# Optimization experiments

Hardware: AMD Instinct MI355X
Metric: run time of the kernel (lower is better)

Reference implementation:

```python
import jax, jax.numpy as jnp
import numpy as np

B, N, NONGT, D, H, PE = 128, 36, 36, 1024, 16, 64
DG = D // H  # per-head dim = 64


def setup_inputs() -> dict:
    key = jax.random.key(0)
    ks = jax.random.split(key, 10)
    s = 0.02
    return {
        "roi_feat": jax.random.normal(ks[0], (B, N, D), jnp.float32),
        "adj_matrix": jax.random.randint(ks[1], (B, N, NONGT), 0, 2, jnp.int32),
        "position_embedding": jax.random.normal(ks[2], (B, N, NONGT, PE), jnp.float32),
        "label_biases_att": jax.random.normal(ks[3], (B, N, NONGT), jnp.float32) * 0.1,
        # effective (weight-normed) linear weights
        "Wq": jax.random.normal(ks[4], (D, D), jnp.float32) * s,
        "bq": jnp.zeros((D,), jnp.float32),
        "Wk": jax.random.normal(ks[5], (D, D), jnp.float32) * s,
        "bk": jnp.zeros((D,), jnp.float32),
        "Wpos": jax.random.normal(ks[6], (H, PE), jnp.float32) * s,
        "bpos": jnp.zeros((H,), jnp.float32),
        # grouped 1x1 conv (groups=H): per-head projection feat_dim -> feat_dim/H
        "Wout": jax.random.normal(ks[7], (H, DG, D), jnp.float32) * s,
        "bout": jnp.zeros((D,), jnp.float32),
    }


def reference(roi_feat, adj_matrix, position_embedding, label_biases_att,
              Wq, bq, Wk, bk, Wpos, bpos, Wout, bout):
    b, n, d = roi_feat.shape
    nongt = adj_matrix.shape[2]
    dg = d // H
    v = roi_feat[:, :nongt, :]                                  # [B,nongt,D]
    q = (roi_feat @ Wq.T + bq).reshape(b, n, H, dg)             # [B,N,H,dg]
    k = (v @ Wk.T + bk).reshape(b, nongt, H, dg)                # [B,nongt,H,dg]
    # scaled QK^T, laid out [B,N,H,nongt] (orig: matmul then transpose(1,2))
    aff = jnp.einsum('bnhd,bmhd->bnhm', q, k) / jnp.sqrt(jnp.float32(dg))
    # position log-bias
    pos = jax.nn.relu(position_embedding.reshape(b, n * nongt, -1) @ Wpos.T + bpos)
    pos = pos.reshape(b, n, nongt, H).transpose(0, 1, 3, 2)     # [B,N,H,nongt]
    waff = aff + jnp.log(jnp.maximum(pos, jnp.float32(1e-6)))
    # adjacency mask + label bias (orig does this in [B,N,nongt,H] layout; equivalent)
    mask = adj_matrix[:, :, None, :] > 0                        # [B,N,1,nongt]
    waff = jnp.where(mask, waff, jnp.float32(-9e15)) + label_biases_att[:, :, None, :]
    att = jax.nn.softmax(waff, axis=-1)                         # [B,N,H,nongt]
    # weighted sum of full V (note: V is full feat_dim per head, not dg)
    out_t = jnp.einsum('bnhm,bmd->bnhd', att, v)                # [B,N,H,D]
    # grouped 1x1 conv: per-head D -> D/H, heads concatenated
    out = jnp.einsum('bnhd,hed->bnhe', out_t, Wout).reshape(b, n, d) + bout
    return out
```

## Files before the change

kernel.cpp:

```cpp
#include <hip/hip_runtime.h>
#include <hip/hip_bf16.h>

#define BB 128
#define NN 36
#define DD 1024
#define HH 16
#define ROWS (BB*NN)

typedef __attribute__((ext_vector_type(8))) __bf16 bf16x8;
typedef __attribute__((ext_vector_type(4))) float f32x4;
typedef __attribute__((ext_vector_type(4))) unsigned short us4;

__device__ inline unsigned short f2bf(float f) {
    __hip_bfloat16 h = __float2bfloat16(f);
    return *reinterpret_cast<unsigned short*>(&h);
}

__device__ inline void async16(const unsigned short* g, unsigned short* l) {
    __builtin_amdgcn_global_load_lds((const __attribute__((address_space(1))) unsigned int*)g,
                                     (__attribute__((address_space(3))) unsigned int*)l, 16, 0, 0);
}

__global__ __launch_bounds__(256) void prep_kernel(const float* __restrict__ roi,
                                                   const float* __restrict__ Wq,
                                                   const float* __restrict__ Wk,
                                                   const float* __restrict__ Wout,
                                                   const float* __restrict__ pe,
                                                   const float* __restrict__ Wpos,
                                                   const float* __restrict__ bpos,
                                                   const int* __restrict__ adj,
                                                   const float* __restrict__ lbl,
                                                   unsigned short* __restrict__ roi_bf,
                                                   unsigned short* __restrict__ Wcat_bf,
                                                   float* __restrict__ extra) {
    const int bid = blockIdx.x, tid = threadIdx.x;
    if (bid < 4608) {
        int i = bid * 256 + tid;
        f32x4 v = ((const f32x4*)roi)[i];
        us4 o;
        o.x = f2bf(v[0]); o.y = f2bf(v[1]); o.z = f2bf(v[2]); o.w = f2bf(v[3]);
        ((us4*)roi_bf)[i] = o;
        return;
    }
    if (bid < 7680) {
        int wb = bid - 4608;
        int sel = wb >> 10;
        const float* src = sel == 0 ? Wq : (sel == 1 ? Wk : Wout);
        int i = (wb & 1023) * 256 + tid;
        f32x4 v = ((const f32x4*)src)[i];
        us4 o;
        o.x = f2bf(v[0]); o.y = f2bf(v[1]); o.z = f2bf(v[2]); o.w = f2bf(v[3]);
        ((us4*)(Wcat_bf + (size_t)sel * DD * DD))[i] = o;
        return;
    }
    __shared__ __align__(16) float wps[HH * 64];
    __shared__ float bps[HH];
    for (int i = tid; i < HH * 64; i += 256) wps[i] = Wpos[i];
    if (tid < HH) bps[tid] = bpos[tid];
    __syncthreads();

    int idx = (bid - 7680) * 256 + tid;
    f32x4 pr[16];
    const f32x4* pv = (const f32x4*)(pe + (size_t)idx * 64);
#pragma unroll
    for (int j = 0; j < 16; j++) pr[j] = pv[j];
    int a = adj[idx];
    float add = lbl[idx] + (a > 0 ? 0.f : -9e15f);
    int b = idx / 1296, nm = idx % 1296;
    size_t obase = (size_t)b * (16 * 1296) + nm;
    for (int hh = 0; hh < 16; hh++) {
        const f32x4* wv = (const f32x4*)(wps + hh * 64);
        f32x4 acc4 = {0.f, 0.f, 0.f, 0.f};
#pragma unroll
        for (int j = 0; j < 16; j++) acc4 += pr[j] * wv[j];
        float d = acc4[0] + acc4[1] + acc4[2] + acc4[3] + bps[hh];
        d = fmaxf(d, 0.f);
        d = __logf(fmaxf(d, 1e-6f));
        extra[obase + (size_t)hh * 1296] = d + add;
    }
}

__global__ __launch_bounds__(256, 2) void fused_kernel(const unsigned short* __restrict__ A,
                                                       const unsigned short* __restrict__ Wc,
                                                       const float* __restrict__ bq,
                                                       const float* __restrict__ bk,
                                                       const float* __restrict__ extra,
                                                       const float* __restrict__ bout,
                                                       float* __restrict__ out) {
    __shared__ __align__(16) unsigned short pool[21504];
    const int tid  = threadIdx.x;
    const int wave = tid >> 6, lane = tid & 63;
    const int quad = lane >> 4, l16 = lane & 15;
    const int h  = blockIdx.x & 15;
    const int bg = blockIdx.x >> 4;
    const int row0 = bg * 144;

    unsigned short* As = pool;
    unsigned short* Bs = pool + 9216;

    const unsigned short* gsrc[11];
    unsigned short* ldst[11];
#pragma unroll
    for (int i = 0; i < 11; i++) {
        int j = wave + 4 * i;
        int c = j * 64 + lane;
        if (j < 18) {
            int row = c >> 3;
            int col = ((c & 7) ^ (row & 7)) * 8;
            gsrc[i] = A + (size_t)(row0 + row) * DD + col;
            ldst[i] = As + j * 512;
        } else {
            int cb = c - 1152;
            int row = cb >> 3;
            int sec = row >> 6;
            int wrow = sec * DD + h * 64 + (row & 63);
            int col = ((cb & 7) ^ (row & 7)) * 8;
            gsrc[i] = Wc + (size_t)wrow * DD + col;
            ldst[i] = Bs + (j - 18) * 512;
        }
    }

    f32x4 acc[9][3] = {};

#pragma unroll
    for (int k0i = 0; k0i < 16; k0i++) {
#pragma unroll
        for (int i = 0; i < 11; i++) {
            if (i < 10 || wave < 2)
                async16(gsrc[i] + k0i * 64, ldst[i]);
        }
        __syncthreads();

#pragma unroll
        for (int ks = 0; ks < 2; ks++) {
            int kch = ks * 4 + quad;
            bf16x8 bfv[3], afv[9];
#pragma unroll
            for (int ct = 0; ct < 3; ct++) {
                int rowb = wave * 48 + ct * 16 + l16;
                bfv[ct] = *(const bf16x8*)&Bs[rowb * 64 + ((kch ^ (rowb & 7)) * 8)];
            }
#pragma unroll
            for (int rt = 0; rt < 9; rt++) {
                int rowa = rt * 16 + l16;
                afv[rt] = *(const bf16x8*)&As[rowa * 64 + ((kch ^ (rowa & 7)) * 8)];
            }
#pragma unroll
            for (int rt = 0; rt < 9; rt++)
#pragma unroll
                for (int ct = 0; ct < 3; ct++)
                    acc[rt][ct] = __builtin_amdgcn_mfma_f32_16x16x32_bf16(afv[rt], bfv[ct], acc[rt][ct], 0, 0, 0);
        }
        __syncthreads();
    }

    const int bat = wave;
    const float* exb = extra + ((size_t)((bg * 4 + bat) * 16 + h)) * 1296;
    float exv[3][4][3];
#pragma unroll
    for (int mt = 0; mt < 3; mt++)
#pragma unroll
        for (int r = 0; r < 4; r++) {
            int row = mt * 16 + quad * 4 + r;
#pragma unroll
            for (int nt = 0; nt < 3; nt++) {
                int col = nt * 16 + l16;
                exv[mt][r][nt] = (row < 36 && col < 36) ? exb[row * 36 + col] : 0.f;
            }
        }
    float bo[4];
#pragma unroll
    for (int nt = 0; nt < 4; nt++) bo[nt] = bout[h * 64 + nt * 16 + l16];

    unsigned short* qL = pool;
    unsigned short* kL = pool + 10368;
#pragma unroll
    for (int ct = 0; ct < 3; ct++) {
        int g = wave * 48 + ct * 16 + l16;
        int sec = g >> 6, e = g & 63;
        if (sec < 2) {
            unsigned short* dst = (sec == 0) ? qL : kL;
            float bias = (sec == 0) ? bq[h * 64 + e] : bk[h * 64 + e];
#pragma unroll
            for (int rt = 0; rt < 9; rt++)
#pragma unroll
                for (int r = 0; r < 4; r++) {
                    int row = rt * 16 + quad * 4 + r;
                    dst[row * 72 + e] = f2bf(acc[rt][ct][r] + bias);
                }
        }
    }
    __syncthreads();

    const unsigned short* qB = qL + bat * 36 * 72;
    const unsigned short* kB = kL + bat * 36 * 72;
    int rq[3];
#pragma unroll
    for (int t = 0; t < 3; t++) { int rr = t * 16 + l16; rq[t] = rr < 36 ? rr : 35; }

    f32x4 aff[3][3] = {};
#pragma unroll
    for (int ks = 0; ks < 2; ks++) {
        bf16x8 afr[3], bfr[3];
#pragma unroll
        for (int t = 0; t < 3; t++) afr[t] = *(const bf16x8*)&qB[rq[t] * 72 + ks * 32 + quad * 8];
#pragma unroll
        for (int t = 0; t < 3; t++) bfr[t] = *(const bf16x8*)&kB[rq[t] * 72 + ks * 32 + quad * 8];
#pragma unroll
        for (int mt = 0; mt < 3; mt++)
#pragma unroll
            for (int nt = 0; nt < 3; nt++)
                aff[mt][nt] = __builtin_amdgcn_mfma_f32_16x16x32_bf16(afr[mt], bfr[nt], aff[mt][nt], 0, 0, 0);
    }
    __syncthreads();

    unsigned short* vwT   = pool;
    unsigned short* attsL = pool + 10240 + bat * 2688;
#pragma unroll
    for (int mt = 0; mt < 3; mt++) {
#pragma unroll
        for (int r = 0; r < 4; r++) {
            int row = mt * 16 + quad * 4 + r;
            float w[3];
#pragma unroll
            for (int nt = 0; nt < 3; nt++) {
                int col = nt * 16 + l16;
                bool valid = (row < 36) && (col < 36);
                w[nt] = valid ? (aff[mt][nt][r] * 0.125f + exv[mt][r][nt]) : -3.4e38f;
            }
            float mx = fmaxf(fmaxf(w[0], w[1]), w[2]);
#pragma unroll
            for (int d = 1; d < 16; d <<= 1) mx = fmaxf(mx, __shfl_xor(mx, d));
            float e0 = __expf(w[0] - mx), e1 = __expf(w[1] - mx), e2 = __expf(w[2] - mx);
            float s = e0 + e1 + e2;
#pragma unroll
            for (int d = 1; d < 16; d <<= 1) s += __shfl_xor(s, d);
            float rs = 1.0f / s;
            attsL[row * 56 + 0  + l16] = f2bf(e0 * rs);
            attsL[row * 56 + 16 + l16] = f2bf(e1 * rs);
            attsL[row * 56 + 32 + l16] = f2bf(e2 * rs);
        }
    }
#pragma unroll
    for (int ct = 0; ct < 3; ct++) {
        int g = wave * 48 + ct * 16 + l16;
        int sec = g >> 6, e = g & 63;
        if (sec == 2) {
#pragma unroll
            for (int rt = 0; rt < 9; rt++)
#pragma unroll
                for (int r = 0; r < 4; r++) {
                    int row = rt * 16 + quad * 4 + r;
                    int bb = row / 36, m = row - bb * 36;
                    vwT[bb * 2560 + e * 40 + m] = f2bf(acc[rt][ct][r]);
                }
        }
    }
    __syncthreads();

    const unsigned short* vB = vwT + bat * 2560;
    f32x4 o[3][4] = {};
    {
        bf16x8 pa[3], pb[4], zf = {};
#pragma unroll
        for (int mt = 0; mt < 3; mt++) pa[mt] = *(const bf16x8*)&attsL[(mt * 16 + l16) * 56 + quad * 8];
#pragma unroll
        for (int nt = 0; nt < 4; nt++) pb[nt] = *(const bf16x8*)&vB[(nt * 16 + l16) * 40 + quad * 8];
#pragma unroll
        for (int mt = 0; mt < 3; mt++)
#pragma unroll
            for (int nt = 0; nt < 4; nt++)
                o[mt][nt] = __builtin_amdgcn_mfma_f32_16x16x32_bf16(pa[mt], pb[nt], o[mt][nt], 0, 0, 0);
#pragma unroll
        for (int mt = 0; mt < 3; mt++)
            pa[mt] = (quad < 2) ? *(const bf16x8*)&attsL[(mt * 16 + l16) * 56 + 32 + quad * 8] : zf;
#pragma unroll
        for (int nt = 0; nt < 4; nt++)
            pb[nt] = (quad < 2) ? *(const bf16x8*)&vB[(nt * 16 + l16) * 40 + 32 + quad * 8] : zf;
#pragma unroll
        for (int mt = 0; mt < 3; mt++)
#pragma unroll
            for (int nt = 0; nt < 4; nt++)
                o[mt][nt] = __builtin_amdgcn_mfma_f32_16x16x32_bf16(pa[mt], pb[nt], o[mt][nt], 0, 0, 0);
    }

    const size_t obase = (size_t)((bg * 4 + bat) * 36) * DD + h * 64;
#pragma unroll
    for (int mt = 0; mt < 3; mt++)
#pragma unroll
        for (int r = 0; r < 4; r++) {
            int n = mt * 16 + quad * 4 + r;
            if (n < 36) {
#pragma unroll
                for (int nt = 0; nt < 4; nt++)
                    out[obase + (size_t)n * DD + nt * 16 + l16] = o[mt][nt][r] + bo[nt];
            }
        }
}

extern "C" void kernel_launch(void* const* d_in, const int* in_sizes, int n_in,
                              void* d_out, int out_size, void* d_ws, size_t ws_size,
                              hipStream_t stream) {
    const float* roi  = (const float*)d_in[0];
    const int*   adj  = (const int*)  d_in[1];
    const float* pe   = (const float*)d_in[2];
    const float* lbl  = (const float*)d_in[3];
    const float* Wq   = (const float*)d_in[4];
    const float* bq   = (const float*)d_in[5];
    const float* Wk   = (const float*)d_in[6];
    const float* bk   = (const float*)d_in[7];
    const float* Wpos = (const float*)d_in[8];
    const float* bpos = (const float*)d_in[9];
    const float* Wout = (const float*)d_in[10];
    const float* bout = (const float*)d_in[11];
    float* out = (float*)d_out;

    char* w = (char*)d_ws;
    unsigned short* roi_bf  = (unsigned short*)(w);
    unsigned short* Wcat_bf = (unsigned short*)(w + 9437184);
    float*          extra   = (float*)(w + 15728640);

    prep_kernel<<<8328, 256, 0, stream>>>(roi, Wq, Wk, Wout, pe, Wpos, bpos, adj, lbl,
                                          roi_bf, Wcat_bf, extra);
    fused_kernel<<<32 * 16, 256, 0, stream>>>(roi_bf, Wcat_bf, bq, bk, extra, bout, out);
}
```

Measured before the change: 173.0 us.

## Double-buffer GEMM main loop with 512-thread blocks covering 8 batches

Each block grows from 256 to 512 threads and now covers 288 rows (8 batches) instead of 144, so the grid halves to 256 blocks. The K loop switches from single-buffer load-sync-compute to double-buffered LDS. Prefetches of the next tile are interleaved with MFMA phases, and the loop uses barriers, waitcnt and s_setprio scheduling hints. The goal is to hide global-to-LDS latency and reuse the weight tile across more rows, at the cost of much larger LDS use and fewer blocks.

Result: slower. 186.9 us (+8.0%).

```diff
diff --git a/kernel.cpp b/kernel.cpp
--- a/kernel.cpp
+++ b/kernel.cpp
@@ -80,82 +80,128 @@
     }
 }
 
-__global__ __launch_bounds__(256, 2) void fused_kernel(const unsigned short* __restrict__ A,
+__global__ __launch_bounds__(512, 2) void fused_kernel(const unsigned short* __restrict__ A,
                                                        const unsigned short* __restrict__ Wc,
                                                        const float* __restrict__ bq,
                                                        const float* __restrict__ bk,
                                                        const float* __restrict__ extra,
                                                        const float* __restrict__ bout,
                                                        float* __restrict__ out) {
-    __shared__ __align__(16) unsigned short pool[21504];
+    __shared__ __align__(16) unsigned short pool[61440];
     const int tid  = threadIdx.x;
     const int wave = tid >> 6, lane = tid & 63;
     const int quad = lane >> 4, l16 = lane & 15;
     const int h  = blockIdx.x & 15;
     const int bg = blockIdx.x >> 4;
-    const int row0 = bg * 144;
-
-    unsigned short* As = pool;
-    unsigned short* Bs = pool + 9216;
-
-    const unsigned short* gsrc[11];
-    unsigned short* ldst[11];
-#pragma unroll
-    for (int i = 0; i < 11; i++) {
-        int j = wave + 4 * i;
-        int c = j * 64 + lane;
-        if (j < 18) {
+    const int row0 = bg * 288;
+    const int wm = wave >> 2, wn = wave & 3;
+    const bool tail = (wave < 4);
+
+    const unsigned short* gsrc[8];
+    int loff[8];
+#pragma unroll
+    for (int i = 0; i < 8; i++) {
+        int j = wave + 8 * i;
+        int jj = j < 60 ? j : 0;
+        int c = jj * 64 + lane;
+        if (jj < 36) {
             int row = c >> 3;
             int col = ((c & 7) ^ (row & 7)) * 8;
             gsrc[i] = A + (size_t)(row0 + row) * DD + col;
-            ldst[i] = As + j * 512;
+            loff[i] = jj * 512;
         } else {
-            int cb = c - 1152;
+            int cb = c - 2304;
             int row = cb >> 3;
             int sec = row >> 6;
             int wrow = sec * DD + h * 64 + (row & 63);
             int col = ((cb & 7) ^ (row & 7)) * 8;
             gsrc[i] = Wc + (size_t)wrow * DD + col;
-            ldst[i] = Bs + (j - 18) * 512;
+            loff[i] = 18432 + (jj - 36) * 512;
         }
     }
 
     f32x4 acc[9][3] = {};
 
 #pragma unroll
-    for (int k0i = 0; k0i < 16; k0i++) {
-#pragma unroll
-        for (int i = 0; i < 11; i++) {
-            if (i < 10 || wave < 2)
-                async16(gsrc[i] + k0i * 64, ldst[i]);
-        }
-        __syncthreads();
-
-#pragma unroll
-        for (int ks = 0; ks < 2; ks++) {
-            int kch = ks * 4 + quad;
-            bf16x8 bfv[3], afv[9];
-#pragma unroll
-            for (int ct = 0; ct < 3; ct++) {
-                int rowb = wave * 48 + ct * 16 + l16;
-                bfv[ct] = *(const bf16x8*)&Bs[rowb * 64 + ((kch ^ (rowb & 7)) * 8)];
-            }
-#pragma unroll
-            for (int rt = 0; rt < 9; rt++) {
-                int rowa = rt * 16 + l16;
-                afv[rt] = *(const bf16x8*)&As[rowa * 64 + ((kch ^ (rowa & 7)) * 8)];
-            }
-#pragma unroll
-            for (int rt = 0; rt < 9; rt++)
-#pragma unroll
-                for (int ct = 0; ct < 3; ct++)
-                    acc[rt][ct] = __builtin_amdgcn_mfma_f32_16x16x32_bf16(afv[rt], bfv[ct], acc[rt][ct], 0, 0, 0);
-        }
-        __syncthreads();
-    }
+    for (int i = 0; i < 7; i++) async16(gsrc[i], pool + loff[i]);
+    if (tail) async16(gsrc[7], pool + loff[7]);
+    asm volatile("s_waitcnt vmcnt(0)" ::: "memory");
+    __builtin_amdgcn_s_barrier();
+
+#define LDB(ct_, kch_) { int rowb = wn * 48 + (ct_) * 16 + l16; \
+    bfv[ct_] = *(const bf16x8*)&cbuf[18432 + rowb * 64 + (((kch_) ^ (rowb & 7)) * 8)]; }
+#define LDA(rt_, kch_) { int rowa = wm * 144 + (rt_) * 16 + l16; \
+    afv[rt_] = *(const bf16x8*)&cbuf[rowa * 64 + (((kch_) ^ (rowa & 7)) * 8)]; }
+#define STAGE(i_) { if ((i_) < 7 || tail) async16(gsrc[i_] + kadv, nbuf + loff[i_]); }
+#define PH_WAIT { __builtin_amdgcn_s_barrier(); \
+    asm volatile("s_waitcnt lgkmcnt(0)" ::: "memory"); \
+    __builtin_amdgcn_sched_barrier(0); }
+
+#pragma unroll 2
+    for (int t = 0; t < 16; ++t) {
+        unsigned short* cbuf = pool + (t & 1) * 30720;
+        unsigned short* nbuf = pool + ((t & 1) ^ 1) * 30720;
+        const int kadv = (t + 1) * 64;
+        const bool pf = (t < 15);
+        bf16x8 bfv[3], afv[9];
+
+        LDB(0, quad) LDB(1, quad) LDB(2, quad)
+        LDA(0, quad) LDA(1, quad) LDA(2, quad) LDA(3, quad) LDA(4, quad)
+        if (pf) { STAGE(0) STAGE(1) STAGE(2) }
+        PH_WAIT;
+        __builtin_amdgcn_s_setprio(1);
+#pragma unroll
+        for (int rt = 0; rt < 5; rt++)
+#pragma unroll
+            for (int ct = 0; ct < 3; ct++)
+                acc[rt][ct] = __builtin_amdgcn_mfma_f32_16x16x32_bf16(afv[rt], bfv[ct], acc[rt][ct], 0, 0, 0);
+        __builtin_amdgcn_s_setprio(0);
+        __builtin_amdgcn_s_barrier();
+
+        LDA(5, quad) LDA(6, quad) LDA(7, quad) LDA(8, quad)
+        if (pf) { STAGE(3) STAGE(4) STAGE(5) }
+        PH_WAIT;
+        __builtin_amdgcn_s_setprio(1);
+#pragma unroll
+        for (int rt = 5; rt < 9; rt++)
+#pragma unroll
+            for (int ct = 0; ct < 3; ct++)
+                acc[rt][ct] = __builtin_amdgcn_mfma_f32_16x16x32_bf16(afv[rt], bfv[ct], acc[rt][ct], 0, 0, 0);
+        __builtin_amdgcn_s_setprio(0);
+        __builtin_amdgcn_s_barrier();
+
+        LDB(0, 4 + quad) LDB(1, 4 + quad) LDB(2, 4 + quad)
+        LDA(0, 4 + quad) LDA(1, 4 + quad) LDA(2, 4 + quad) LDA(3, 4 + quad) LDA(4, 4 + quad)
+        if (pf) { STAGE(6) STAGE(7) }
+        PH_WAIT;
+        __builtin_amdgcn_s_setprio(1);
+#pragma unroll
+        for (int rt = 0; rt < 5; rt++)
+#pragma unroll
+            for (int ct = 0; ct < 3; ct++)
+                acc[rt][ct] = __builtin_amdgcn_mfma_f32_16x16x32_bf16(afv[rt], bfv[ct], acc[rt][ct], 0, 0, 0);
+        __builtin_amdgcn_s_setprio(0);
+        __builtin_amdgcn_s_barrier();
+
+        LDA(5, 4 + quad) LDA(6, 4 + quad) LDA(7, 4 + quad) LDA(8, 4 + quad)
+        PH_WAIT;
+        __builtin_amdgcn_s_setprio(1);
+#pragma unroll
+        for (int rt = 5; rt < 9; rt++)
+#pragma unroll
+            for (int ct = 0; ct < 3; ct++)
+                acc[rt][ct] = __builtin_amdgcn_mfma_f32_16x16x32_bf16(afv[rt], bfv[ct], acc[rt][ct], 0, 0, 0);
+        __builtin_amdgcn_s_setprio(0);
+        asm volatile("s_waitcnt vmcnt(0)" ::: "memory");
+        __builtin_amdgcn_s_barrier();
+    }
+#undef LDB
+#undef LDA
+#undef STAGE
+#undef PH_WAIT
 
     const int bat = wave;
-    const float* exb = extra + ((size_t)((bg * 4 + bat) * 16 + h)) * 1296;
+    const float* exb = extra + ((size_t)((bg * 8 + bat) * 16 + h)) * 1296;
     float exv[3][4][3];
 #pragma unroll
     for (int mt = 0; mt < 3; mt++)
@@ -173,10 +219,10 @@
     for (int nt = 0; nt < 4; nt++) bo[nt] = bout[h * 64 + nt * 16 + l16];
 
     unsigned short* qL = pool;
-    unsigned short* kL = pool + 10368;
+    unsigned short* kL = pool + 20736;
 #pragma unroll
     for (int ct = 0; ct < 3; ct++) {
-        int g = wave * 48 + ct * 16 + l16;
+        int g = wn * 48 + ct * 16 + l16;
         int sec = g >> 6, e = g & 63;
         if (sec < 2) {
             unsigned short* dst = (sec == 0) ? qL : kL;
@@ -185,7 +231,7 @@
             for (int rt = 0; rt < 9; rt++)
 #pragma unroll
                 for (int r = 0; r < 4; r++) {
-                    int row = rt * 16 + quad * 4 + r;
+                    int row = wm * 144 + rt * 16 + quad * 4 + r;
                     dst[row * 72 + e] = f2bf(acc[rt][ct][r] + bias);
                 }
         }
@@ -215,7 +261,7 @@
     __syncthreads();
 
     unsigned short* vwT   = pool;
-    unsigned short* attsL = pool + 10240 + bat * 2688;
+    unsigned short* attsL = pool + 20480 + bat * 2688;
 #pragma unroll
     for (int mt = 0; mt < 3; mt++) {
 #pragma unroll
@@ -243,14 +289,14 @@
     }
 #pragma unroll
     for (int ct = 0; ct < 3; ct++) {
-        int g = wave * 48 + ct * 16 + l16;
+        int g = wn * 48 + ct * 16 + l16;
         int sec = g >> 6, e = g & 63;
         if (sec == 2) {
 #pragma unroll
             for (int rt = 0; rt < 9; rt++)
 #pragma unroll
                 for (int r = 0; r < 4; r++) {
-                    int row = rt * 16 + quad * 4 + r;
+                    int row = wm * 144 + rt * 16 + quad * 4 + r;
                     int bb = row / 36, m = row - bb * 36;
                     vwT[bb * 2560 + e * 40 + m] = f2bf(acc[rt][ct][r]);
                 }
@@ -284,7 +330,7 @@
                 o[mt][nt] = __builtin_amdgcn_mfma_f32_16x16x32_bf16(pa[mt], pb[nt], o[mt][nt], 0, 0, 0);
     }
 
-    const size_t obase = (size_t)((bg * 4 + bat) * 36) * DD + h * 64;
+    const size_t obase = (size_t)((bg * 8 + bat) * 36) * DD + h * 64;
 #pragma unroll
     for (int mt = 0; mt < 3; mt++)
 #pragma unroll
@@ -322,5 +368,5 @@
 
     prep_kernel<<<8328, 256, 0, stream>>>(roi, Wq, Wk, Wout, pe, Wpos, bpos, adj, lbl,
                                           roi_bf, Wcat_bf, extra);
-    fused_kernel<<<32 * 16, 256, 0, stream>>>(roi_bf, Wcat_bf, bq, bk, extra, bout, out);
-}
+    fused_kernel<<<16 * 16, 512, 0, stream>>>(roi_bf, Wcat_bf, bq, bk, extra, bout, out);
+}
```

## Double-buffer GEMM K-loop with 32-wide K tiles and async prefetch

Applied to the files above, without the earlier changes.

The main GEMM loop moves from single-buffered 64-wide K tiles, which synchronised twice per step and stalled on every load, to double-buffered 32-wide K tiles. The next tile is issued with async global-to-LDS loads while MFMAs run on the current one. The LDS swizzle is adapted to the narrower rows, and s_setprio is raised around the MFMA block. The cost is twice as many iterations and barriers, and it relies on the 32-wide layout being conflict-free.

Result: faster. 168.6 us (-2.6%).

```diff
diff --git a/kernel.cpp b/kernel.cpp
--- a/kernel.cpp
+++ b/kernel.cpp
@@ -95,62 +95,64 @@
     const int bg = blockIdx.x >> 4;
     const int row0 = bg * 144;
 
-    unsigned short* As = pool;
-    unsigned short* Bs = pool + 9216;
-
-    const unsigned short* gsrc[11];
-    unsigned short* ldst[11];
-#pragma unroll
-    for (int i = 0; i < 11; i++) {
+    const unsigned short* gsrc[6];
+    int loff[6];
+#pragma unroll
+    for (int i = 0; i < 6; i++) {
         int j = wave + 4 * i;
-        int c = j * 64 + lane;
-        if (j < 18) {
-            int row = c >> 3;
-            int col = ((c & 7) ^ (row & 7)) * 8;
+        int jj = j < 21 ? j : 0;
+        int c = jj * 64 + lane;
+        if (jj < 9) {
+            int row = c >> 2, cc = c & 3;
+            int col = (cc ^ ((row >> 1) & 3)) * 8;
             gsrc[i] = A + (size_t)(row0 + row) * DD + col;
-            ldst[i] = As + j * 512;
+            loff[i] = jj * 512;
         } else {
-            int cb = c - 1152;
-            int row = cb >> 3;
+            int cb = c - 576;
+            int row = cb >> 2, cc = cb & 3;
             int sec = row >> 6;
             int wrow = sec * DD + h * 64 + (row & 63);
-            int col = ((cb & 7) ^ (row & 7)) * 8;
+            int col = (cc ^ ((row >> 1) & 3)) * 8;
             gsrc[i] = Wc + (size_t)wrow * DD + col;
-            ldst[i] = Bs + (j - 18) * 512;
+            loff[i] = 4608 + (jj - 9) * 512;
         }
     }
 
     f32x4 acc[9][3] = {};
 
 #pragma unroll
-    for (int k0i = 0; k0i < 16; k0i++) {
-#pragma unroll
-        for (int i = 0; i < 11; i++) {
-            if (i < 10 || wave < 2)
-                async16(gsrc[i] + k0i * 64, ldst[i]);
-        }
-        __syncthreads();
-
-#pragma unroll
-        for (int ks = 0; ks < 2; ks++) {
-            int kch = ks * 4 + quad;
-            bf16x8 bfv[3], afv[9];
-#pragma unroll
-            for (int ct = 0; ct < 3; ct++) {
-                int rowb = wave * 48 + ct * 16 + l16;
-                bfv[ct] = *(const bf16x8*)&Bs[rowb * 64 + ((kch ^ (rowb & 7)) * 8)];
-            }
-#pragma unroll
-            for (int rt = 0; rt < 9; rt++) {
-                int rowa = rt * 16 + l16;
-                afv[rt] = *(const bf16x8*)&As[rowa * 64 + ((kch ^ (rowa & 7)) * 8)];
-            }
-#pragma unroll
-            for (int rt = 0; rt < 9; rt++)
-#pragma unroll
-                for (int ct = 0; ct < 3; ct++)
-                    acc[rt][ct] = __builtin_amdgcn_mfma_f32_16x16x32_bf16(afv[rt], bfv[ct], acc[rt][ct], 0, 0, 0);
-        }
+    for (int i = 0; i < 6; i++)
+        if (i < 5 || wave == 0) async16(gsrc[i], pool + loff[i]);
+    __syncthreads();
+
+#pragma unroll 2
+    for (int t = 0; t < 32; ++t) {
+        unsigned short* cbuf = pool + (t & 1) * 10752;
+        unsigned short* nbuf = pool + ((t & 1) ^ 1) * 10752;
+        if (t < 31) {
+            const int kadv = (t + 1) * 32;
+#pragma unroll
+            for (int i = 0; i < 6; i++)
+                if (i < 5 || wave == 0) async16(gsrc[i] + kadv, nbuf + loff[i]);
+        }
+        bf16x8 bfv[3], afv[9];
+#pragma unroll
+        for (int ct = 0; ct < 3; ct++) {
+            int rowb = wave * 48 + ct * 16 + l16;
+            bfv[ct] = *(const bf16x8*)&cbuf[4608 + rowb * 32 + ((quad ^ ((rowb >> 1) & 3)) * 8)];
+        }
+#pragma unroll
+        for (int rt = 0; rt < 9; rt++) {
+            int rowa = rt * 16 + l16;
+            afv[rt] = *(const bf16x8*)&cbuf[rowa * 32 + ((quad ^ ((rowa >> 1) & 3)) * 8)];
+        }
+        __builtin_amdgcn_s_setprio(1);
+#pragma unroll
+        for (int rt = 0; rt < 9; rt++)
+#pragma unroll
+            for (int ct = 0; ct < 3; ct++)
+                acc[rt][ct] = __builtin_amdgcn_mfma_f32_16x16x32_bf16(afv[rt], bfv[ct], acc[rt][ct], 0, 0, 0);
+        __builtin_amdgcn_s_setprio(0);
         __syncthreads();
     }
 
```
